# Kernel optimization log

Measured on AMD Instinct MI355X. Metric: run time of the kernel, lower is better.

## Reference

```python
import jax, jax.numpy as jnp
import numpy as np

H = 256            # hidden_size
N_NODE = 50000     # item vocab
NUM_GRAPHS = 4096
NODES_PER_G = 20
EDGES_PER_G = 40
N = NUM_GRAPHS * NODES_PER_G      # 81920
E = NUM_GRAPHS * EDGES_PER_G      # 163840


def setup_inputs() -> dict:
    key = jax.random.key(0)
    ks = jax.random.split(key, 16)
    stdv = 1.0 / np.sqrt(H)
    u = lambda k, shape: jax.random.uniform(k, shape, jnp.float32, -stdv, stdv)

    # graph data: 1-based item ids, sorted batch vector, within-graph edges
    x = jax.random.randint(ks[0], (N,), 1, N_NODE, dtype=jnp.int64)
    batch = jnp.repeat(jnp.arange(NUM_GRAPHS, dtype=jnp.int64), NODES_PER_G)
    base = jnp.repeat(jnp.arange(NUM_GRAPHS, dtype=jnp.int64) * NODES_PER_G, EDGES_PER_G)
    src = base + jax.random.randint(ks[1], (E,), 0, NODES_PER_G, dtype=jnp.int64)
    dst = base + jax.random.randint(ks[2], (E,), 0, NODES_PER_G, dtype=jnp.int64)
    edge_index = jnp.stack([src, dst])

    return {
        "x": x, "edge_index": edge_index, "batch": batch,
        "emb": u(ks[3], (N_NODE, H)),
        "gated_w": u(ks[4], (2, H, H)),      # GatedGraphConv weight, num_layers=2
        "w_ih": u(ks[5], (3 * H, H)), "w_hh": u(ks[6], (3 * H, H)),
        "b_ih": u(ks[7], (3 * H,)), "b_hh": u(ks[8], (3 * H,)),
        "W1": u(ks[9], (H, H)), "b1": u(ks[10], (H,)),
        "W2": u(ks[11], (H, H)), "b2": u(ks[12], (H,)),
        "qw": u(ks[13], (1, H)), "qb": u(ks[14], (1,)),
        "W3": u(ks[15], (H, 2 * H)), "b3": jnp.zeros((H,), jnp.float32),
    }


def _forward(x, edge_index, batch, emb, gated_w, w_ih, w_hh, b_ih, b_hh,
             W1, b1, W2, b2, qw, qb, W3, b3):
    h = emb[x - 1]                                   # [N, H] embedding lookup
    src, dst = edge_index[0], edge_index[1]

    # GatedGraphConv: 2 layers of (linear -> scatter-add over edges -> GRUCell)
    for i in range(2):
        m = h @ gated_w[i]                           # [N, H]
        agg = jnp.zeros_like(h).at[dst].add(m[src])  # message aggregation
        gi = agg @ w_ih.T + b_ih                     # GRU input gates
        gh = h @ w_hh.T + b_hh                       # GRU hidden gates
        i_r, i_z, i_n = jnp.split(gi, 3, axis=-1)
        h_r, h_z, h_n = jnp.split(gh, 3, axis=-1)
        r = jax.nn.sigmoid(i_r + h_r)
        z = jax.nn.sigmoid(i_z + h_z)
        n = jnp.tanh(i_n + r * h_n)
        h = (1.0 - z) * n + z * h

    # Embedding2Score: last-node attention readout per graph
    counts = jnp.bincount(batch, length=NUM_GRAPHS)          # [B]
    last_idx = jnp.cumsum(counts) - 1                        # last node of each graph
    v_n = h[last_idx]                                        # [B, H]
    alpha = jax.nn.sigmoid(v_n[batch] @ W1.T + b1 + h @ W2.T + b2) @ qw.T + qb  # [N, 1]
    s_g = jax.ops.segment_sum(alpha * h, batch, num_segments=NUM_GRAPHS)        # [B, H]
    s_h = jnp.concatenate([v_n, s_g], axis=-1) @ W3.T + b3                      # [B, H]
    return s_h @ emb.T                                       # [B, N_NODE] scores


def reference(x, edge_index, batch, emb, gated_w, w_ih, w_hh, b_ih, b_hh,
              W1, b1, W2, b2, qw, qb, W3, b3):
    return _forward(x, edge_index, batch, emb, gated_w, w_ih, w_hh, b_ih, b_hh,
                    W1, b1, W2, b2, qw, qb, W3, b3)
```

## Files before the change

kernel.cpp:

```cpp
#include <hip/hip_runtime.h>

typedef __attribute__((ext_vector_type(8))) __bf16 bf16x8;
typedef __attribute__((ext_vector_type(4))) float f32x4;

#define DEV __device__ __forceinline__

DEV unsigned short f2bf(float f) {
  unsigned u = __float_as_uint(f);
  u = (u + 0x7fffu + ((u >> 16) & 1u)) >> 16;
  return (unsigned short)u;
}
DEV float bf2f(unsigned short s) { return __uint_as_float(((unsigned)s) << 16); }
DEV float sigm(float x) { return 1.f / (1.f + expf(-x)); }

DEV uint4 pack8(f32x4 a, f32x4 b) {
  uint4 o;
  o.x = (unsigned)f2bf(a[0]) | ((unsigned)f2bf(a[1]) << 16);
  o.y = (unsigned)f2bf(a[2]) | ((unsigned)f2bf(a[3]) << 16);
  o.z = (unsigned)f2bf(b[0]) | ((unsigned)f2bf(b[1]) << 16);
  o.w = (unsigned)f2bf(b[2]) | ((unsigned)f2bf(b[3]) << 16);
  return o;
}

#define GL16(SRC, LDSB)                                                                    \
  __builtin_amdgcn_global_load_lds(                                                       \
      (const __attribute__((address_space(1))) unsigned int*)(SRC),                       \
      (__attribute__((address_space(3))) unsigned int*)(LDSB), 16, 0, 0)

template<int MODE, bool BIAS>
__global__ __launch_bounds__(256)
void gemm_bt(const unsigned short* __restrict__ A, const unsigned short* __restrict__ Bm,
             const float* __restrict__ bias, void* __restrict__ Cv,
             const float* __restrict__ vw1, const float* __restrict__ qwf,
             const int* __restrict__ batchp, int M, int N, int K)
{
  __shared__ unsigned short sm[16384];
  unsigned short* As = sm;
  unsigned short* Bs = sm + 8192;

  const int tid  = threadIdx.x;
  const int lane = tid & 63;
  const int wv   = tid >> 6;
  const int wr   = (wv >> 1) << 6;
  const int wc   = (wv & 1) << 6;
  const long mTile = (long)blockIdx.y << 7;
  const long nTile = (long)blockIdx.x << 7;

  const f32x4 z4 = {0.f, 0.f, 0.f, 0.f};
  f32x4 acc[4][4];
  #pragma unroll
  for (int i = 0; i < 4; ++i)
    #pragma unroll
    for (int j = 0; j < 4; ++j) acc[i][j] = z4;

  const int crow = lane >> 3;
  const int ckb  = (lane & 7) << 4;

  for (int k0 = 0; k0 < K; k0 += 64) {
    #pragma unroll
    for (int i = 0; i < 4; ++i) {
      const int c   = (wv << 2) + i;
      const int row = (c << 3) + crow;
      const int kb  = ckb ^ ((row & 7) << 4);
      const unsigned short* sA = A + (mTile + row) * K + k0 + (kb >> 1);
      GL16(sA, (char*)As + (c << 10));
      int bn = (int)nTile + row; bn = bn < N ? bn : (N - 1);
      const unsigned short* sB = Bm + (long)bn * K + k0 + (kb >> 1);
      GL16(sB, (char*)Bs + (c << 10));
    }
    __syncthreads();
    #pragma unroll
    for (int kk = 0; kk < 64; kk += 32) {
      const int kbl = (kk + ((lane >> 4) << 3)) << 1;
      bf16x8 af[4], bfv[4];
      #pragma unroll
      for (int mi = 0; mi < 4; ++mi) {
        const int rr = wr + (mi << 4) + (lane & 15);
        af[mi] = *(const bf16x8*)((const char*)As + (rr << 7) + (kbl ^ ((rr & 7) << 4)));
      }
      #pragma unroll
      for (int ni = 0; ni < 4; ++ni) {
        const int rr = wc + (ni << 4) + (lane & 15);
        bfv[ni] = *(const bf16x8*)((const char*)Bs + (rr << 7) + (kbl ^ ((rr & 7) << 4)));
      }
      #pragma unroll
      for (int mi = 0; mi < 4; ++mi)
        #pragma unroll
        for (int ni = 0; ni < 4; ++ni)
          acc[mi][ni] = __builtin_amdgcn_mfma_f32_16x16x32_bf16(af[mi], bfv[ni], acc[mi][ni], 0, 0, 0);
    }
    __syncthreads();
  }

  if constexpr (MODE == 2) {
    const int slice = (int)blockIdx.x * 2 + (wc >> 6);
    #pragma unroll
    for (int mi = 0; mi < 4; ++mi) {
      #pragma unroll
      for (int j = 0; j < 4; ++j) {
        const long row = mTile + wr + (mi << 4) + ((lane >> 4) << 2) + j;
        const long vb = (long)batchp[row] << 8;
        float part = 0.f;
        #pragma unroll
        for (int ni = 0; ni < 4; ++ni) {
          const int col = (int)nTile + wc + (ni << 4) + (lane & 15);
          part += sigm(acc[mi][ni][j] + vw1[vb + col]) * qwf[col];
        }
        #pragma unroll
        for (int off = 1; off < 16; off <<= 1) part += __shfl_xor(part, off, 64);
        if ((lane & 15) == 0) ((float*)Cv)[(long)slice * M + row] = part;
      }
    }
  } else {
    #pragma unroll
    for (int ni = 0; ni < 4; ++ni) {
      const long col = nTile + wc + (ni << 4) + (lane & 15);
      if (col < N) {
        float bv = 0.f;
        if constexpr (BIAS) bv = bias[col];
        #pragma unroll
        for (int mi = 0; mi < 4; ++mi) {
          const long row = mTile + wr + (mi << 4) + ((lane >> 4) << 2);
          #pragma unroll
          for (int j = 0; j < 4; ++j) {
            const float v = acc[mi][ni][j] + bv;
            if constexpr (MODE == 1) ((unsigned short*)Cv)[(row + j) * N + col] = f2bf(v);
            else                     ((float*)Cv)[(row + j) * N + col] = v;
          }
        }
      }
    }
  }
}

__global__ __launch_bounds__(512, 2)
void k_ggru(const unsigned short* __restrict__ agg, const unsigned short* __restrict__ hin,
            const unsigned short* __restrict__ wihb, const unsigned short* __restrict__ whhb,
            const float* __restrict__ bih, const float* __restrict__ bhh,
            unsigned short* __restrict__ hout)
{
  extern __shared__ unsigned short sm[];
  const int tid  = threadIdx.x;
  const int lane = tid & 63;
  const int wv   = tid >> 6;
  const int rh   = wv >> 2;
  const int cg   = wv & 3;
  const int D0   = blockIdx.x << 6;
  const long mTile = (long)blockIdx.y << 7;

  const f32x4 z4 = {0.f, 0.f, 0.f, 0.f};
  f32x4 acc[4][6];
  #pragma unroll
  for (int i = 0; i < 4; ++i)
    #pragma unroll
    for (int g = 0; g < 6; ++g) acc[i][g] = z4;

  const int crow = lane >> 3;
  const int ckb  = (lane & 7) << 4;

  for (int k0 = 0; k0 < 256; k0 += 64) {
    #pragma unroll
    for (int i = 0; i < 10; ++i) {
      const int c = wv * 10 + i;
      if (c < 32) {
        const unsigned short* src = (c < 16) ? agg : hin;
        const int row = ((c & 15) << 3) + crow;
        const int kb  = ckb ^ ((row & 7) << 4);
        GL16(src + (mTile + row) * 256 + k0 + (kb >> 1), (char*)sm + (c << 10));
      } else {
        const int g  = (c - 32) >> 3;
        const int lr = (((c - 32) & 7) << 3) + crow;
        const unsigned short* Ws = (g < 3) ? wihb : whhb;
        const long grow = (long)((g % 3) * 256 + D0 + lr);
        const int kb = ckb ^ ((lr & 7) << 4);
        GL16(Ws + grow * 256 + k0 + (kb >> 1), (char*)sm + (c << 10));
      }
    }
    __syncthreads();
    #pragma unroll
    for (int kk = 0; kk < 64; kk += 32) {
      const int kbl = (kk + ((lane >> 4) << 3)) << 1;
      bf16x8 fa[4], fh[4], fb[6];
      #pragma unroll
      for (int mi = 0; mi < 4; ++mi) {
        const int r = (rh << 6) + (mi << 4) + (lane & 15);
        const int off = (r << 7) + (kbl ^ ((r & 7) << 4));
        fa[mi] = *(const bf16x8*)((const char*)sm + off);
        fh[mi] = *(const bf16x8*)((const char*)sm + 16384 + off);
      }
      const int lr = (cg << 4) + (lane & 15);
      const int boff = (lr << 7) + (kbl ^ ((lr & 7) << 4));
      #pragma unroll
      for (int g = 0; g < 6; ++g)
        fb[g] = *(const bf16x8*)((const char*)sm + 32768 + (g << 13) + boff);
      #pragma unroll
      for (int mi = 0; mi < 4; ++mi) {
        #pragma unroll
        for (int g = 0; g < 3; ++g)
          acc[mi][g] = __builtin_amdgcn_mfma_f32_16x16x32_bf16(fa[mi], fb[g], acc[mi][g], 0, 0, 0);
        #pragma unroll
        for (int g = 3; g < 6; ++g)
          acc[mi][g] = __builtin_amdgcn_mfma_f32_16x16x32_bf16(fh[mi], fb[g], acc[mi][g], 0, 0, 0);
      }
    }
    __syncthreads();
  }

  const int d = D0 + (cg << 4) + (lane & 15);
  const float bir = bih[d], biz = bih[256 + d], bin_ = bih[512 + d];
  const float bhr = bhh[d], bhz = bhh[256 + d], bhn  = bhh[512 + d];
  #pragma unroll
  for (int mi = 0; mi < 4; ++mi) {
    #pragma unroll
    for (int j = 0; j < 4; ++j) {
      const long row = mTile + (rh << 6) + (mi << 4) + ((lane >> 4) << 2) + j;
      const float hold = bf2f(hin[row * 256 + d]);
      const float r  = sigm(acc[mi][0][j] + bir + acc[mi][3][j] + bhr);
      const float z  = sigm(acc[mi][1][j] + biz + acc[mi][4][j] + bhz);
      const float n  = tanhf(acc[mi][2][j] + bin_ + r * (acc[mi][5][j] + bhn));
      hout[row * 256 + d] = f2bf((1.f - z) * n + z * hold);
    }
  }
}

__global__ void k_cvt8(const float* __restrict__ in, unsigned short* __restrict__ out, long n8)
{
  const long i = (long)blockIdx.x * 256 + threadIdx.x;
  if (i >= n8) return;
  const f32x4 a = *(const f32x4*)(in + i * 8);
  const f32x4 b = *(const f32x4*)(in + i * 8 + 4);
  *(uint4*)(out + i * 8) = pack8(a, b);
}

__global__ void k_tr(const float* __restrict__ g, unsigned short* __restrict__ o)
{
  const int mat = blockIdx.x >> 8;
  const int n   = blockIdx.x & 255;
  const int k   = threadIdx.x;
  o[mat * 65536 + n * 256 + k] = f2bf(g[mat * 65536 + k * 256 + n]);
}

__global__ void k_b12(const float* __restrict__ b1, const float* __restrict__ b2,
                      float* __restrict__ o)
{
  o[threadIdx.x] = b1[threadIdx.x] + b2[threadIdx.x];
}

__global__ void k_gather(const int* __restrict__ x, const float* __restrict__ emb,
                         unsigned short* __restrict__ h)
{
  const long i = (long)blockIdx.x * 256 + threadIdx.x;
  const long node = i >> 5;
  const int  d0 = ((int)i & 31) << 3;
  const long row = (long)x[node] - 1;
  const float* p = emb + row * 256 + d0;
  const f32x4 a = *(const f32x4*)p;
  const f32x4 b = *(const f32x4*)(p + 4);
  *(uint4*)(h + node * 256 + d0) = pack8(a, b);
}

__global__ void k_scatter(const unsigned short* __restrict__ m, const int* __restrict__ ei,
                          unsigned short* __restrict__ agg, int E)
{
  __shared__ float aggs[20 * 256];
  __shared__ int es[40], ed[40];
  const int g = blockIdx.x;
  const int d = threadIdx.x;
  if (d < 40) es[d] = ei[g * 40 + d];
  if (d >= 128 && d < 168) ed[d - 128] = ei[E + g * 40 + (d - 128)];
  #pragma unroll
  for (int i = 0; i < 20; ++i) aggs[i * 256 + d] = 0.f;
  __syncthreads();
  for (int e = 0; e < 40; ++e) {
    const float mv = bf2f(m[(long)es[e] * 256 + d]);
    const int loc = ed[e] - g * 20;
    aggs[loc * 256 + d] += mv;
  }
  const long base = (long)g * (20 * 256);
  #pragma unroll
  for (int i = 0; i < 20; ++i)
    agg[base + i * 256 + d] = f2bf(aggs[i * 256 + d]);
}

__global__ void k_lastidx(const int* __restrict__ batch, int* __restrict__ last, int n, int ng)
{
  const int g = blockIdx.x * blockDim.x + threadIdx.x;
  if (g >= ng) return;
  int lo = 0, hi = n;
  while (lo < hi) { const int mid = (lo + hi) >> 1; if (batch[mid] > g) hi = mid; else lo = mid + 1; }
  last[g] = lo - 1;
}

__global__ void k_vn(const unsigned short* __restrict__ h, const int* __restrict__ last,
                     unsigned short* __restrict__ vn, unsigned short* __restrict__ cat)
{
  const long i = (long)blockIdx.x * 256 + threadIdx.x;
  const long g = i >> 5;
  const int  d0 = ((int)i & 31) << 3;
  const uint4 v = *(const uint4*)(h + (long)last[g] * 256 + d0);
  *(uint4*)(vn + g * 256 + d0) = v;
  *(uint4*)(cat + g * 512 + d0) = v;
}

__global__ void k_sg(const float* __restrict__ alph2, const float* __restrict__ qb,
                     const unsigned short* __restrict__ h, unsigned short* __restrict__ cat, int Nn)
{
  __shared__ float al[20];
  const int g = blockIdx.x, d = threadIdx.x;
  if (d < 20) {
    const int n = g * 20 + d;
    al[d] = qb[0] + alph2[n] + alph2[Nn + n] + alph2[2 * Nn + n] + alph2[3 * Nn + n];
  }
  __syncthreads();
  float s = 0.f;
  const unsigned short* hp = h + (long)g * 20 * 256 + d;
  #pragma unroll
  for (int i = 0; i < 20; ++i) s += al[i] * bf2f(hp[i * 256]);
  cat[(long)g * 512 + 256 + d] = f2bf(s);
}

extern "C" void kernel_launch(void* const* d_in, const int* in_sizes, int n_in,
                              void* d_out, int out_size, void* d_ws, size_t ws_size,
                              hipStream_t stream)
{
  const int*   x     = (const int*)  d_in[0];
  const int*   ei    = (const int*)  d_in[1];
  const int*   batch = (const int*)  d_in[2];
  const float* emb   = (const float*)d_in[3];
  const float* gw    = (const float*)d_in[4];
  const float* wih   = (const float*)d_in[5];
  const float* whh   = (const float*)d_in[6];
  const float* bih   = (const float*)d_in[7];
  const float* bhh   = (const float*)d_in[8];
  const float* W1    = (const float*)d_in[9];
  const float* b1    = (const float*)d_in[10];
  const float* W2    = (const float*)d_in[11];
  const float* b2    = (const float*)d_in[12];
  const float* qw    = (const float*)d_in[13];
  const float* qb    = (const float*)d_in[14];
  const float* W3    = (const float*)d_in[15];
  const float* b3    = (const float*)d_in[16];

  const int Nn = in_sizes[0];
  const int E  = in_sizes[1] / 2;
  const int V  = in_sizes[3] / 256;
  const int B  = out_size / V;

  char* w = (char*)d_ws;
  auto take = [&](size_t bytes) { char* r = w; w += (bytes + 1023) & ~(size_t)1023; return r; };
  unsigned short* h_   = (unsigned short*)take((size_t)Nn * 256 * 2);
  unsigned short* m_   = (unsigned short*)take((size_t)Nn * 256 * 2);
  unsigned short* agg_ = (unsigned short*)take((size_t)Nn * 256 * 2);
  unsigned short* embb = (unsigned short*)take((size_t)V * 256 * 2);
  unsigned short* gtw  = (unsigned short*)take((size_t)2 * 65536 * 2);
  unsigned short* wihb = (unsigned short*)take((size_t)768 * 256 * 2);
  unsigned short* whhb = (unsigned short*)take((size_t)768 * 256 * 2);
  unsigned short* w1b  = (unsigned short*)take((size_t)65536 * 2);
  unsigned short* w2b  = (unsigned short*)take((size_t)65536 * 2);
  unsigned short* w3b  = (unsigned short*)take((size_t)131072 * 2);
  unsigned short* vnb  = (unsigned short*)take((size_t)B * 256 * 2);
  unsigned short* catb = (unsigned short*)take((size_t)B * 512 * 2);
  unsigned short* shb  = (unsigned short*)take((size_t)B * 256 * 2);
  float*          b12  = (float*)take(256 * 4);
  int*            last = (int*)take((size_t)B * 4);
  float*          alph2= (float*)take((size_t)4 * Nn * 4);
  float*          vw1  = (float*)take((size_t)B * 256 * 4);

  const int MBn = Nn / 128;
  const int MBb = B / 128;
  const int NBv = (V + 127) / 128;

  k_cvt8<<<dim3(((long)V * 256 / 8 + 255) / 256), 256, 0, stream>>>(emb, embb, (long)V * 256 / 8);
  k_tr  <<<dim3(512), 256, 0, stream>>>(gw, gtw);
  k_cvt8<<<dim3(96),  256, 0, stream>>>(wih, wihb, 768 * 256 / 8);
  k_cvt8<<<dim3(96),  256, 0, stream>>>(whh, whhb, 768 * 256 / 8);
  k_cvt8<<<dim3(32),  256, 0, stream>>>(W1, w1b, 65536 / 8);
  k_cvt8<<<dim3(32),  256, 0, stream>>>(W2, w2b, 65536 / 8);
  k_cvt8<<<dim3(64),  256, 0, stream>>>(W3, w3b, 131072 / 8);
  k_b12 <<<dim3(1),   256, 0, stream>>>(b1, b2, b12);
  k_gather<<<dim3(Nn * 32 / 256), 256, 0, stream>>>(x, emb, h_);

  unsigned short* hc = h_;
  unsigned short* mb = m_;
  for (int L = 0; L < 2; ++L) {
    gemm_bt<1, false><<<dim3(2, MBn), 256, 0, stream>>>(hc, gtw + (size_t)L * 65536, nullptr, mb,
                                                        nullptr, nullptr, nullptr, Nn, 256, 256);
    k_scatter<<<dim3(B), 256, 0, stream>>>(mb, ei, agg_, E);
    k_ggru<<<dim3(4, MBn), 512, 81920, stream>>>(agg_, hc, wihb, whhb, bih, bhh, mb);
    unsigned short* t = hc; hc = mb; mb = t;
  }

  k_lastidx<<<dim3((B + 255) / 256), 256, 0, stream>>>(batch, last, Nn, B);
  k_vn<<<dim3(B * 32 / 256), 256, 0, stream>>>(hc, last, vnb, catb);
  gemm_bt<0, true><<<dim3(2, MBb), 256, 0, stream>>>(vnb, w1b, b12, vw1,
                                                     nullptr, nullptr, nullptr, B, 256, 256);
  gemm_bt<2, false><<<dim3(2, MBn), 256, 0, stream>>>(hc, w2b, nullptr, alph2,
                                                      vw1, qw, batch, Nn, 256, 256);
  k_sg<<<dim3(B), 256, 0, stream>>>(alph2, qb, hc, catb, Nn);
  gemm_bt<1, true><<<dim3(2, MBb), 256, 0, stream>>>(catb, w3b, b3, shb,
                                                     nullptr, nullptr, nullptr, B, 256, 512);

  gemm_bt<0, false><<<dim3(NBv, MBb), 256, 0, stream>>>(shb, embb, nullptr, (float*)d_out,
                                                        nullptr, nullptr, nullptr, B, V, 256);

  (void)n_in; (void)ws_size;
}
```

Before: 830.7 us.

## Double-buffer GRU kernel LDS, fuse prep launches, swap final GEMM grid order

The GRU gate kernel now double-buffers its LDS stages (160KB dynamic shared memory) so the next K-slice loads while the current one is computed, and it drops the 2-blocks-per-CU launch bound. The weight conversion, transpose and bias-sum kernels are merged into one prep launch, and last-index lookup is folded into k_vn. The final score GEMM swaps grid axes so consecutive blocks share the same embedding tile for better L2 reuse. The larger LDS footprint limits GRU occupancy to one block per CU.

```diff
diff --git a/kernel.cpp b/kernel.cpp
--- a/kernel.cpp
+++ b/kernel.cpp
@@ -27,7 +27,7 @@
       (const __attribute__((address_space(1))) unsigned int*)(SRC),                       \
       (__attribute__((address_space(3))) unsigned int*)(LDSB), 16, 0, 0)
 
-template<int MODE, bool BIAS>
+template<int MODE, bool BIAS, bool XM>
 __global__ __launch_bounds__(256)
 void gemm_bt(const unsigned short* __restrict__ A, const unsigned short* __restrict__ Bm,
              const float* __restrict__ bias, void* __restrict__ Cv,
@@ -43,8 +43,10 @@
   const int wv   = tid >> 6;
   const int wr   = (wv >> 1) << 6;
   const int wc   = (wv & 1) << 6;
-  const long mTile = (long)blockIdx.y << 7;
-  const long nTile = (long)blockIdx.x << 7;
+  const int nBlk = XM ? blockIdx.y : blockIdx.x;
+  const int mBlk = XM ? blockIdx.x : blockIdx.y;
+  const long mTile = (long)mBlk << 7;
+  const long nTile = (long)nBlk << 7;
 
   const f32x4 z4 = {0.f, 0.f, 0.f, 0.f};
   f32x4 acc[4][4];
@@ -93,7 +95,7 @@
   }
 
   if constexpr (MODE == 2) {
-    const int slice = (int)blockIdx.x * 2 + (wc >> 6);
+    const int slice = nBlk * 2 + (wc >> 6);
     #pragma unroll
     for (int mi = 0; mi < 4; ++mi) {
       #pragma unroll
@@ -133,13 +135,13 @@
   }
 }
 
-__global__ __launch_bounds__(512, 2)
+__global__ __launch_bounds__(512)
 void k_ggru(const unsigned short* __restrict__ agg, const unsigned short* __restrict__ hin,
             const unsigned short* __restrict__ wihb, const unsigned short* __restrict__ whhb,
             const float* __restrict__ bih, const float* __restrict__ bhh,
             unsigned short* __restrict__ hout)
 {
-  extern __shared__ unsigned short sm[];
+  extern __shared__ unsigned short smd[];
   const int tid  = threadIdx.x;
   const int lane = tid & 63;
   const int wv   = tid >> 6;
@@ -158,7 +160,8 @@
   const int crow = lane >> 3;
   const int ckb  = (lane & 7) << 4;
 
-  for (int k0 = 0; k0 < 256; k0 += 64) {
+  auto stage = [&](int buf, int k0) {
+    char* base = (char*)smd + buf * 81920;
     #pragma unroll
     for (int i = 0; i < 10; ++i) {
       const int c = wv * 10 + i;
@@ -166,17 +169,24 @@
         const unsigned short* src = (c < 16) ? agg : hin;
         const int row = ((c & 15) << 3) + crow;
         const int kb  = ckb ^ ((row & 7) << 4);
-        GL16(src + (mTile + row) * 256 + k0 + (kb >> 1), (char*)sm + (c << 10));
+        GL16(src + (mTile + row) * 256 + k0 + (kb >> 1), base + (c << 10));
       } else {
         const int g  = (c - 32) >> 3;
         const int lr = (((c - 32) & 7) << 3) + crow;
         const unsigned short* Ws = (g < 3) ? wihb : whhb;
         const long grow = (long)((g % 3) * 256 + D0 + lr);
         const int kb = ckb ^ ((lr & 7) << 4);
-        GL16(Ws + grow * 256 + k0 + (kb >> 1), (char*)sm + (c << 10));
-      }
-    }
-    __syncthreads();
+        GL16(Ws + grow * 256 + k0 + (kb >> 1), base + (c << 10));
+      }
+    }
+  };
+
+  stage(0, 0);
+  __syncthreads();
+  int cur = 0;
+  for (int t = 0; t < 4; ++t) {
+    if (t < 3) stage(cur ^ 1, (t + 1) << 6);
+    const char* bb = (const char*)smd + cur * 81920;
     #pragma unroll
     for (int kk = 0; kk < 64; kk += 32) {
       const int kbl = (kk + ((lane >> 4) << 3)) << 1;
@@ -185,14 +195,14 @@
       for (int mi = 0; mi < 4; ++mi) {
         const int r = (rh << 6) + (mi << 4) + (lane & 15);
         const int off = (r << 7) + (kbl ^ ((r & 7) << 4));
-        fa[mi] = *(const bf16x8*)((const char*)sm + off);
-        fh[mi] = *(const bf16x8*)((const char*)sm + 16384 + off);
+        fa[mi] = *(const bf16x8*)(bb + off);
+        fh[mi] = *(const bf16x8*)(bb + 16384 + off);
       }
       const int lr = (cg << 4) + (lane & 15);
       const int boff = (lr << 7) + (kbl ^ ((lr & 7) << 4));
       #pragma unroll
       for (int g = 0; g < 6; ++g)
-        fb[g] = *(const bf16x8*)((const char*)sm + 32768 + (g << 13) + boff);
+        fb[g] = *(const bf16x8*)(bb + 32768 + (g << 13) + boff);
       #pragma unroll
       for (int mi = 0; mi < 4; ++mi) {
         #pragma unroll
@@ -204,6 +214,7 @@
       }
     }
     __syncthreads();
+    cur ^= 1;
   }
 
   const int d = D0 + (cg << 4) + (lane & 15);
@@ -232,18 +243,38 @@
   *(uint4*)(out + i * 8) = pack8(a, b);
 }
 
-__global__ void k_tr(const float* __restrict__ g, unsigned short* __restrict__ o)
-{
-  const int mat = blockIdx.x >> 8;
-  const int n   = blockIdx.x & 255;
-  const int k   = threadIdx.x;
-  o[mat * 65536 + n * 256 + k] = f2bf(g[mat * 65536 + k * 256 + n]);
-}
-
-__global__ void k_b12(const float* __restrict__ b1, const float* __restrict__ b2,
-                      float* __restrict__ o)
-{
-  o[threadIdx.x] = b1[threadIdx.x] + b2[threadIdx.x];
+__global__ void k_prep(const float* __restrict__ wih, const float* __restrict__ whh,
+                       const float* __restrict__ W1, const float* __restrict__ W2,
+                       const float* __restrict__ W3, const float* __restrict__ b1,
+                       const float* __restrict__ b2, const float* __restrict__ gw,
+                       unsigned short* __restrict__ wihb, unsigned short* __restrict__ whhb,
+                       unsigned short* __restrict__ w1b, unsigned short* __restrict__ w2b,
+                       unsigned short* __restrict__ w3b, float* __restrict__ b12,
+                       unsigned short* __restrict__ gtw)
+{
+  const int b = blockIdx.x, t = threadIdx.x;
+  if (b < 256) {
+    const float* src; unsigned short* dst; int base;
+    if (b < 96)       { src = wih; dst = wihb; base = b; }
+    else if (b < 192) { src = whh; dst = whhb; base = b - 96; }
+    else if (b < 224) { src = W1;  dst = w1b;  base = b - 192; }
+    else              { src = W2;  dst = w2b;  base = b - 224; }
+    const long i = (long)base * 256 + t;
+    const f32x4 a = *(const f32x4*)(src + i * 8);
+    const f32x4 c = *(const f32x4*)(src + i * 8 + 4);
+    *(uint4*)(dst + i * 8) = pack8(a, c);
+  } else if (b < 320) {
+    const long i = (long)(b - 256) * 256 + t;
+    const f32x4 a = *(const f32x4*)(W3 + i * 8);
+    const f32x4 c = *(const f32x4*)(W3 + i * 8 + 4);
+    *(uint4*)(w3b + i * 8) = pack8(a, c);
+  } else if (b == 320) {
+    b12[t] = b1[t] + b2[t];
+  } else {
+    const int bb = b - 321;
+    const int mat = bb >> 8, n = bb & 255;
+    gtw[mat * 65536 + n * 256 + t] = f2bf(gw[mat * 65536 + t * 256 + n]);
+  }
 }
 
 __global__ void k_gather(const int* __restrict__ x, const float* __restrict__ emb,
@@ -282,22 +313,15 @@
     agg[base + i * 256 + d] = f2bf(aggs[i * 256 + d]);
 }
 
-__global__ void k_lastidx(const int* __restrict__ batch, int* __restrict__ last, int n, int ng)
-{
-  const int g = blockIdx.x * blockDim.x + threadIdx.x;
-  if (g >= ng) return;
-  int lo = 0, hi = n;
-  while (lo < hi) { const int mid = (lo + hi) >> 1; if (batch[mid] > g) hi = mid; else lo = mid + 1; }
-  last[g] = lo - 1;
-}
-
-__global__ void k_vn(const unsigned short* __restrict__ h, const int* __restrict__ last,
-                     unsigned short* __restrict__ vn, unsigned short* __restrict__ cat)
+__global__ void k_vn(const unsigned short* __restrict__ h, const int* __restrict__ batch,
+                     unsigned short* __restrict__ vn, unsigned short* __restrict__ cat, int n)
 {
   const long i = (long)blockIdx.x * 256 + threadIdx.x;
   const long g = i >> 5;
   const int  d0 = ((int)i & 31) << 3;
-  const uint4 v = *(const uint4*)(h + (long)last[g] * 256 + d0);
+  int lo = 0, hi = n;
+  while (lo < hi) { const int mid = (lo + hi) >> 1; if (batch[mid] > (int)g) hi = mid; else lo = mid + 1; }
+  const uint4 v = *(const uint4*)(h + (long)(lo - 1) * 256 + d0);
   *(uint4*)(vn + g * 256 + d0) = v;
   *(uint4*)(cat + g * 512 + d0) = v;
 }
@@ -362,7 +386,6 @@
   unsigned short* catb = (unsigned short*)take((size_t)B * 512 * 2);
   unsigned short* shb  = (unsigned short*)take((size_t)B * 256 * 2);
   float*          b12  = (float*)take(256 * 4);
-  int*            last = (int*)take((size_t)B * 4);
   float*          alph2= (float*)take((size_t)4 * Nn * 4);
   float*          vw1  = (float*)take((size_t)B * 256 * 4);
 
@@ -370,38 +393,35 @@
   const int MBb = B / 128;
   const int NBv = (V + 127) / 128;
 
+  (void)hipFuncSetAttribute((const void*)k_ggru,
+                            hipFuncAttributeMaxDynamicSharedMemorySize, 163840);
+
   k_cvt8<<<dim3(((long)V * 256 / 8 + 255) / 256), 256, 0, stream>>>(emb, embb, (long)V * 256 / 8);
-  k_tr  <<<dim3(512), 256, 0, stream>>>(gw, gtw);
-  k_cvt8<<<dim3(96),  256, 0, stream>>>(wih, wihb, 768 * 256 / 8);
-  k_cvt8<<<dim3(96),  256, 0, stream>>>(whh, whhb, 768 * 256 / 8);
-  k_cvt8<<<dim3(32),  256, 0, stream>>>(W1, w1b, 65536 / 8);
-  k_cvt8<<<dim3(32),  256, 0, stream>>>(W2, w2b, 65536 / 8);
-  k_cvt8<<<dim3(64),  256, 0, stream>>>(W3, w3b, 131072 / 8);
-  k_b12 <<<dim3(1),   256, 0, stream>>>(b1, b2, b12);
+  k_prep<<<dim3(833), 256, 0, stream>>>(wih, whh, W1, W2, W3, b1, b2, gw,
+                                        wihb, whhb, w1b, w2b, w3b, b12, gtw);
   k_gather<<<dim3(Nn * 32 / 256), 256, 0, stream>>>(x, emb, h_);
 
   unsigned short* hc = h_;
   unsigned short* mb = m_;
   for (int L = 0; L < 2; ++L) {
-    gemm_bt<1, false><<<dim3(2, MBn), 256, 0, stream>>>(hc, gtw + (size_t)L * 65536, nullptr, mb,
-                                                        nullptr, nullptr, nullptr, Nn, 256, 256);
+    gemm_bt<1, false, false><<<dim3(2, MBn), 256, 0, stream>>>(hc, gtw + (size_t)L * 65536, nullptr, mb,
+                                                               nullptr, nullptr, nullptr, Nn, 256, 256);
     k_scatter<<<dim3(B), 256, 0, stream>>>(mb, ei, agg_, E);
-    k_ggru<<<dim3(4, MBn), 512, 81920, stream>>>(agg_, hc, wihb, whhb, bih, bhh, mb);
+    k_ggru<<<dim3(4, MBn), 512, 163840, stream>>>(agg_, hc, wihb, whhb, bih, bhh, mb);
     unsigned short* t = hc; hc = mb; mb = t;
   }
 
-  k_lastidx<<<dim3((B + 255) / 256), 256, 0, stream>>>(batch, last, Nn, B);
-  k_vn<<<dim3(B * 32 / 256), 256, 0, stream>>>(hc, last, vnb, catb);
-  gemm_bt<0, true><<<dim3(2, MBb), 256, 0, stream>>>(vnb, w1b, b12, vw1,
-                                                     nullptr, nullptr, nullptr, B, 256, 256);
-  gemm_bt<2, false><<<dim3(2, MBn), 256, 0, stream>>>(hc, w2b, nullptr, alph2,
-                                                      vw1, qw, batch, Nn, 256, 256);
+  k_vn<<<dim3(B * 32 / 256), 256, 0, stream>>>(hc, batch, vnb, catb, Nn);
+  gemm_bt<0, true, false><<<dim3(2, MBb), 256, 0, stream>>>(vnb, w1b, b12, vw1,
+                                                            nullptr, nullptr, nullptr, B, 256, 256);
+  gemm_bt<2, false, false><<<dim3(2, MBn), 256, 0, stream>>>(hc, w2b, nullptr, alph2,
+                                                             vw1, qw, batch, Nn, 256, 256);
   k_sg<<<dim3(B), 256, 0, stream>>>(alph2, qb, hc, catb, Nn);
-  gemm_bt<1, true><<<dim3(2, MBb), 256, 0, stream>>>(catb, w3b, b3, shb,
-                                                     nullptr, nullptr, nullptr, B, 256, 512);
-
-  gemm_bt<0, false><<<dim3(NBv, MBb), 256, 0, stream>>>(shb, embb, nullptr, (float*)d_out,
-                                                        nullptr, nullptr, nullptr, B, V, 256);
+  gemm_bt<1, true, false><<<dim3(2, MBb), 256, 0, stream>>>(catb, w3b, b3, shb,
+                                                            nullptr, nullptr, nullptr, B, 256, 512);
+
+  gemm_bt<0, false, true><<<dim3(MBb, NBv), 256, 0, stream>>>(shb, embb, nullptr, (float*)d_out,
+                                                              nullptr, nullptr, nullptr, B, V, 256);
 
   (void)n_in; (void)ws_size;
 }
```

Result: slower. 1.299 ms (+56.4%).
